# Kernel optimization log

Measured on AMD Instinct MI355X. Metric: run time of the kernel, lower is better.

Reference implementation:

```python
import jax, jax.numpy as jnp
import numpy as np

D_MODEL = 1024
NUM_HEADS = 16
D_K = D_MODEL // NUM_HEADS


def setup_inputs() -> dict:
    key = jax.random.key(0)
    ks = jax.random.split(key, 9)
    s = 1.0 / np.sqrt(D_MODEL)
    x = jax.random.normal(ks[0], (4, 2048, D_MODEL), dtype=jnp.float32)
    Wq = jax.random.uniform(ks[1], (D_MODEL, D_MODEL), jnp.float32, -s, s)
    bq = jax.random.uniform(ks[2], (D_MODEL,), jnp.float32, -s, s)
    Wk = jax.random.uniform(ks[3], (D_MODEL, D_MODEL), jnp.float32, -s, s)
    bk = jax.random.uniform(ks[4], (D_MODEL,), jnp.float32, -s, s)
    Wv = jax.random.uniform(ks[5], (D_MODEL, D_MODEL), jnp.float32, -s, s)
    bv = jax.random.uniform(ks[6], (D_MODEL,), jnp.float32, -s, s)
    Wo = jax.random.uniform(ks[7], (D_MODEL, D_MODEL), jnp.float32, -s, s)
    bo = jax.random.uniform(ks[8], (D_MODEL,), jnp.float32, -s, s)
    return {"x": x, "Wq": Wq, "bq": bq, "Wk": Wk, "bk": bk,
            "Wv": Wv, "bv": bv, "Wo": Wo, "bo": bo}


def reference(x, Wq, bq, Wk, bk, Wv, bv, Wo, bo):
    B, S, _ = x.shape
    # project and split heads: [B,S,D] -> [B,H,S,dk]
    def heads(W, b):
        return (x @ W + b).reshape(B, S, NUM_HEADS, D_K).transpose(0, 2, 1, 3)
    q = heads(Wq, bq)
    k = heads(Wk, bk)
    v = heads(Wv, bv)
    scores = jnp.einsum('bhqd,bhkd->bhqk', q, k) / jnp.sqrt(jnp.float32(D_K))
    attn = jax.nn.softmax(scores, axis=-1)
    out = jnp.einsum('bhqk,bhkd->bhqd', attn, v)
    out = out.transpose(0, 2, 1, 3).reshape(B, S, D_MODEL)
    return out @ Wo + bo
```

## Files before the change

### kernel.cpp

```cpp
#include <hip/hip_runtime.h>
#include <hip/hip_bf16.h>

#define D_MODEL 1024
#define NUM_HEADS 16
#define D_K 64
#define B_SZ 4
#define SEQ 2048
#define SCALE_Q 0.180336881f

typedef short bf16x8 __attribute__((ext_vector_type(8)));
typedef float f32x4 __attribute__((ext_vector_type(4)));
typedef unsigned short u16;

__device__ __forceinline__ unsigned cvtpk(float a, float b) {
    unsigned r;
    asm("v_cvt_pk_bf16_f32 %0, %1, %2" : "=v"(r) : "v"(a), "v"(b));
    return r;
}
__device__ __forceinline__ u16 f2bf(float f) {
    return (u16)cvtpk(f, f);
}
__device__ __forceinline__ float exp2a(float x) {
    float r;
    asm("v_exp_f32 %0, %1" : "=v"(r) : "v"(x));
    return r;
}
__device__ __forceinline__ float max3f(float a, float b, float c) {
    float r;
    asm("v_max3_f32 %0, %1, %2, %3" : "=v"(r) : "v"(a), "v"(b), "v"(c));
    return r;
}
__device__ __forceinline__ void gload_lds16(const u16* g, u16* l) {
    __builtin_amdgcn_global_load_lds(
        (const __attribute__((address_space(1))) unsigned int*)g,
        (__attribute__((address_space(3))) unsigned int*)l, 16, 0, 0);
}

__global__ __launch_bounds__(256) void prep_all(
    const float* __restrict__ xin, u16* __restrict__ xbf,
    const float* __restrict__ W0, const float* __restrict__ W1,
    const float* __restrict__ W2, const float* __restrict__ W3,
    u16* __restrict__ Wt)
{
    __shared__ float tile[64][65];
    const int t = threadIdx.x;
    if (blockIdx.x < 1024) {
        const int n8 = (B_SZ * SEQ * D_MODEL) / 8;
        for (int i = blockIdx.x * 256 + t; i < n8; i += 1024 * 256) {
            float4 a = ((const float4*)xin)[(size_t)i * 2];
            float4 b = ((const float4*)xin)[(size_t)i * 2 + 1];
            uint4 o;
            o.x = cvtpk(a.x, a.y);
            o.y = cvtpk(a.z, a.w);
            o.z = cvtpk(b.x, b.y);
            o.w = cvtpk(b.z, b.w);
            ((uint4*)xbf)[i] = o;
        }
        return;
    }
    const int id = blockIdx.x - 1024;
    const int z  = id >> 8;
    const int by = (id >> 4) & 15;
    const int bx = id & 15;
    const float* W = z == 0 ? W0 : z == 1 ? W1 : z == 2 ? W2 : W3;
    u16* out = Wt + (size_t)z * D_MODEL * D_MODEL;
    const int k0 = by * 64;
    const int n0 = bx * 64;
    #pragma unroll
    for (int it = 0; it < 4; ++it) {
        int idx = it * 256 + t;
        int r = idx >> 4;
        int c = (idx & 15) * 4;
        float4 v = *(const float4*)(W + (size_t)(k0 + r) * D_MODEL + n0 + c);
        tile[r][c + 0] = v.x; tile[r][c + 1] = v.y;
        tile[r][c + 2] = v.z; tile[r][c + 3] = v.w;
    }
    __syncthreads();
    #pragma unroll
    for (int it = 0; it < 2; ++it) {
        int idx = it * 256 + t;
        int r = idx >> 3;
        int c = (idx & 7) * 8;
        uint4 o;
        o.x = cvtpk(tile[c + 0][r], tile[c + 1][r]);
        o.y = cvtpk(tile[c + 2][r], tile[c + 3][r]);
        o.z = cvtpk(tile[c + 4][r], tile[c + 5][r]);
        o.w = cvtpk(tile[c + 6][r], tile[c + 7][r]);
        *(uint4*)(out + (size_t)(n0 + r) * D_MODEL + k0 + c) = o;
    }
}

__global__ __launch_bounds__(256) void gemm_qkv(
    const u16* __restrict__ A, const u16* __restrict__ Wt,
    const float* __restrict__ bq, const float* __restrict__ bk,
    const float* __restrict__ bv, u16* __restrict__ Yb)
{
    __shared__ u16 As[2][128][64];
    __shared__ u16 Bs[2][128][64];
    const int t    = threadIdx.x;
    const int lane = t & 63;
    const int wv   = t >> 6;
    const int wm   = wv >> 1, wn = wv & 1;
    const int g    = lane >> 4;
    const int lr   = lane & 15;
    const int fid  = blockIdx.y * 24 + blockIdx.x;
    const int oid  = (fid & 7) * 192 + (fid >> 3);
    const int m0   = (oid / 24) * 128;
    const int n0   = (oid % 24) * 128;
    const int K    = D_MODEL;

    const int srow = lane >> 3;
    const int scol = (lane & 7) * 8;

    f32x4 acc[4][4];
    #pragma unroll
    for (int i = 0; i < 4; ++i)
        #pragma unroll
        for (int j = 0; j < 4; ++j)
            acc[i][j] = (f32x4){0.f, 0.f, 0.f, 0.f};

    #pragma unroll
    for (int it = 0; it < 4; ++it) {
        const int r = wv * 32 + it * 8;
        gload_lds16(A  + (size_t)(m0 + r + srow) * K + scol, &As[0][r][0]);
        gload_lds16(Wt + (size_t)(n0 + r + srow) * K + scol, &Bs[0][r][0]);
    }

    for (int k0 = 0; k0 < K; k0 += 64) {
        const int cur = (k0 >> 6) & 1;
        __syncthreads();
        if (k0 + 64 < K) {
            const int nb = cur ^ 1;
            #pragma unroll
            for (int it = 0; it < 4; ++it) {
                const int r = wv * 32 + it * 8;
                gload_lds16(A  + (size_t)(m0 + r + srow) * K + k0 + 64 + scol, &As[nb][r][0]);
                gload_lds16(Wt + (size_t)(n0 + r + srow) * K + k0 + 64 + scol, &Bs[nb][r][0]);
            }
        }
        #pragma unroll
        for (int s = 0; s < 2; ++s) {
            bf16x8 af[4], bfr[4];
            #pragma unroll
            for (int mt = 0; mt < 4; ++mt)
                af[mt] = *(const bf16x8*)(&As[cur][wm * 64 + mt * 16 + lr][g * 8 + s * 32]);
            #pragma unroll
            for (int nt = 0; nt < 4; ++nt)
                bfr[nt] = *(const bf16x8*)(&Bs[cur][wn * 64 + nt * 16 + lr][g * 8 + s * 32]);
            #pragma unroll
            for (int mt = 0; mt < 4; ++mt)
                #pragma unroll
                for (int nt = 0; nt < 4; ++nt)
                    acc[mt][nt] = __builtin_amdgcn_mfma_f32_16x16x32_bf16(
                        af[mt], bfr[nt], acc[mt][nt], 0, 0, 0);
        }
    }

    const int which = n0 >> 10;
    const float scale = (which == 0) ? SCALE_Q : 1.0f;
    const float* bp = (which == 0) ? bq : (which == 1) ? bk : bv;
    u16* dst = Yb + (size_t)which * ((size_t)B_SZ * SEQ * D_MODEL);

    float bv4[4];
    #pragma unroll
    for (int nt = 0; nt < 4; ++nt)
        bv4[nt] = bp[((n0 + wn * 64 + nt * 16 + lr) & 1023)];

    #pragma unroll
    for (int mt = 0; mt < 4; ++mt) {
        #pragma unroll
        for (int nt = 0; nt < 4; ++nt) {
            float v4[4];
            #pragma unroll
            for (int r = 0; r < 4; ++r) v4[r] = (acc[mt][nt][r] + bv4[nt]) * scale;
            const int mbase = m0 + wm * 64 + mt * 16 + g * 4;
            const int nn = (n0 + wn * 64 + nt * 16 + lr) & 1023;
            const int h = nn >> 6, d = nn & 63;
            const int bb = mbase >> 11, s2 = mbase & 2047;
            if (which == 2) {
                const int z  = s2 & 63;
                const int zp = (z & 32) + 8 * ((z & 15) >> 2) + 4 * ((z >> 4) & 1);
                const int col = zp ^ ((d & 7) << 3);
                uint2 o;
                o.x = cvtpk(v4[0], v4[1]);
                o.y = cvtpk(v4[2], v4[3]);
                *(uint2*)&dst[(((size_t)(bb * NUM_HEADS + h) * D_K + d) * SEQ) + (s2 & ~63) + col] = o;
            } else {
                #pragma unroll
                for (int r = 0; r < 4; ++r) {
                    const int s2r = s2 + r;
                    const int dd = (which == 1) ? (d ^ ((s2r & 7) << 3)) : d;
                    dst[(((size_t)(bb * NUM_HEADS + h) * SEQ) + s2r) * D_K + dd] = f2bf(v4[r]);
                }
            }
        }
    }
}

__global__ __launch_bounds__(256) void gemm_o(
    const u16* __restrict__ A, const u16* __restrict__ Wt,
    const float* __restrict__ bias, float* __restrict__ Y)
{
    __shared__ u16 As[2][128][64];
    __shared__ u16 Bs[2][128][64];
    const int t    = threadIdx.x;
    const int lane = t & 63;
    const int wv   = t >> 6;
    const int wm   = wv >> 1, wn = wv & 1;
    const int g    = lane >> 4;
    const int lr   = lane & 15;
    const int fid  = blockIdx.y * 8 + blockIdx.x;
    const int oid  = (fid & 7) * 64 + (fid >> 3);
    const int m0   = (oid >> 3) * 128;
    const int n0   = (oid & 7) * 128;
    const int K    = D_MODEL;

    const int srow = lane >> 3;
    const int scol = (lane & 7) * 8;

    f32x4 acc[4][4];
    #pragma unroll
    for (int i = 0; i < 4; ++i)
        #pragma unroll
        for (int j = 0; j < 4; ++j)
            acc[i][j] = (f32x4){0.f, 0.f, 0.f, 0.f};

    #pragma unroll
    for (int it = 0; it < 4; ++it) {
        const int r = wv * 32 + it * 8;
        gload_lds16(A  + (size_t)(m0 + r + srow) * K + scol, &As[0][r][0]);
        gload_lds16(Wt + (size_t)(n0 + r + srow) * K + scol, &Bs[0][r][0]);
    }

    for (int k0 = 0; k0 < K; k0 += 64) {
        const int cur = (k0 >> 6) & 1;
        __syncthreads();
        if (k0 + 64 < K) {
            const int nb = cur ^ 1;
            #pragma unroll
            for (int it = 0; it < 4; ++it) {
                const int r = wv * 32 + it * 8;
                gload_lds16(A  + (size_t)(m0 + r + srow) * K + k0 + 64 + scol, &As[nb][r][0]);
                gload_lds16(Wt + (size_t)(n0 + r + srow) * K + k0 + 64 + scol, &Bs[nb][r][0]);
            }
        }
        #pragma unroll
        for (int s = 0; s < 2; ++s) {
            bf16x8 af[4], bfr[4];
            #pragma unroll
            for (int mt = 0; mt < 4; ++mt)
                af[mt] = *(const bf16x8*)(&As[cur][wm * 64 + mt * 16 + lr][g * 8 + s * 32]);
            #pragma unroll
            for (int nt = 0; nt < 4; ++nt)
                bfr[nt] = *(const bf16x8*)(&Bs[cur][wn * 64 + nt * 16 + lr][g * 8 + s * 32]);
            #pragma unroll
            for (int mt = 0; mt < 4; ++mt)
                #pragma unroll
                for (int nt = 0; nt < 4; ++nt)
                    acc[mt][nt] = __builtin_amdgcn_mfma_f32_16x16x32_bf16(
                        af[mt], bfr[nt], acc[mt][nt], 0, 0, 0);
        }
    }

    float bv4[4];
    #pragma unroll
    for (int nt = 0; nt < 4; ++nt) bv4[nt] = bias[n0 + wn * 64 + nt * 16 + lr];

    #pragma unroll
    for (int mt = 0; mt < 4; ++mt)
        #pragma unroll
        for (int nt = 0; nt < 4; ++nt)
            #pragma unroll
            for (int r = 0; r < 4; ++r) {
                const int m = m0 + wm * 64 + mt * 16 + g * 4 + r;
                const int n = n0 + wn * 64 + nt * 16 + lr;
                Y[(size_t)m * D_MODEL + n] = acc[mt][nt][r] + bv4[nt];
            }
}

__global__ __launch_bounds__(512, 4) void attn_mfma(
    const u16* __restrict__ Q, const u16* __restrict__ Kb,
    const u16* __restrict__ Vt, u16* __restrict__ ctx)
{
    __shared__ u16 Ks[2][128][64];
    __shared__ u16 Vs[2][64][128];
    const int t    = threadIdx.x;
    const int lane = t & 63;
    const int w    = t >> 6;
    const int g    = lane >> 4;
    const int lr   = lane & 15;
    const int fid  = blockIdx.x + (blockIdx.y << 3) + (blockIdx.z << 7);
    const int oid  = (fid & 7) * 64 + (fid >> 3);
    const int qt   = oid & 7;
    const int h    = (oid >> 3) & 15;
    const int b    = oid >> 7;
    const size_t hoff = ((size_t)b * NUM_HEADS + h) * SEQ * D_K;

    bf16x8 qf[2][2];
    #pragma unroll
    for (int u = 0; u < 2; ++u) {
        const int q = qt * 256 + w * 32 + u * 16 + lr;
        qf[u][0] = *(const bf16x8*)(Q + hoff + (size_t)q * D_K + g * 8);
        qf[u][1] = *(const bf16x8*)(Q + hoff + (size_t)q * D_K + g * 8 + 32);
    }

    const int krow = w * 16 + (lane >> 3);
    const int kcol = (lane & 7) * 8;
    const u16* ksrc = Kb + hoff + (size_t)krow * D_K + kcol;
    const int vrow = w * 8 + (lane >> 4);
    const int vcol = (lane & 15) * 8;
    const u16* vsrc = Vt + hoff + (size_t)vrow * SEQ + vcol;

    const int xm = (lr & 7) << 3;

    float mrun[2]  = {0.f, 0.f};
    float lpart[2] = {0.f, 0.f};
    f32x4 acc_o[2][4];
    #pragma unroll
    for (int u = 0; u < 2; ++u)
        #pragma unroll
        for (int n = 0; n < 4; ++n) acc_o[u][n] = (f32x4){0.f, 0.f, 0.f, 0.f};

    gload_lds16(ksrc,               &Ks[0][w * 16][0]);
    gload_lds16(ksrc + 8 * D_K,     &Ks[0][w * 16 + 8][0]);
    gload_lds16(vsrc,               &Vs[0][w * 8][0]);
    gload_lds16(vsrc + 4 * SEQ,     &Vs[0][w * 8 + 4][0]);

    int bu = 0;
    for (int kt = 0; kt < SEQ / 128; ++kt) {
        __syncthreads();
        if (kt + 1 < SEQ / 128) {
            const size_t kv0 = (size_t)(kt + 1) * 128;
            const int nb = bu ^ 1;
            gload_lds16(ksrc + kv0 * D_K,       &Ks[nb][w * 16][0]);
            gload_lds16(ksrc + (kv0 + 8) * D_K, &Ks[nb][w * 16 + 8][0]);
            gload_lds16(vsrc + kv0,             &Vs[nb][w * 8][0]);
            gload_lds16(vsrc + 4 * SEQ + kv0,   &Vs[nb][w * 8 + 4][0]);
        }

        #pragma unroll
        for (int hv = 0; hv < 2; ++hv) {
            f32x4 sc[2][4];
            #pragma unroll
            for (int u = 0; u < 2; ++u) {
                const f32x4 mi = {-mrun[u], -mrun[u], -mrun[u], -mrun[u]};
                #pragma unroll
                for (int mt = 0; mt < 4; ++mt) sc[u][mt] = mi;
            }
            __builtin_amdgcn_s_setprio(1);
            #pragma unroll
            for (int s = 0; s < 2; ++s)
                #pragma unroll
                for (int mt = 0; mt < 4; ++mt) {
                    bf16x8 kf = *(const bf16x8*)(
                        &Ks[bu][hv * 64 + mt * 16 + lr][(g * 8 + s * 32) ^ xm]);
                    sc[0][mt] = __builtin_amdgcn_mfma_f32_16x16x32_bf16(kf, qf[0][s], sc[0][mt], 0, 0, 0);
                    sc[1][mt] = __builtin_amdgcn_mfma_f32_16x16x32_bf16(kf, qf[1][s], sc[1][mt], 0, 0, 0);
                }
            __builtin_amdgcn_s_setprio(0);

            union { bf16x8 v; unsigned u[4]; } pa[2][2];
            #pragma unroll
            for (int u = 0; u < 2; ++u) {
                float t0 = max3f(sc[u][0][0], sc[u][0][1], sc[u][0][2]);
                float t1 = max3f(sc[u][0][3], sc[u][1][0], sc[u][1][1]);
                float t2 = max3f(sc[u][1][2], sc[u][1][3], sc[u][2][0]);
                float t3 = max3f(sc[u][2][1], sc[u][2][2], sc[u][2][3]);
                float t4 = max3f(sc[u][3][0], sc[u][3][1], sc[u][3][2]);
                float tmax = fmaxf(max3f(t0, t1, t2), max3f(t3, t4, sc[u][3][3]));

                if (!__all(tmax <= 8.0f)) {
                    float rowmax = fmaxf(tmax, __shfl_xor(tmax, 16));
                    rowmax = fmaxf(rowmax, __shfl_xor(rowmax, 32));
                    const float excess = fmaxf(rowmax, 0.0f);
                    const float alpha = exp2a(-excess);
                    mrun[u] += excess;
                    lpart[u] *= alpha;
                    float ar[4];
                    #pragma unroll
                    for (int r = 0; r < 4; ++r) ar[r] = __shfl(alpha, g * 4 + r);
                    #pragma unroll
                    for (int n = 0; n < 4; ++n) {
                        f32x4 v = acc_o[u][n];
                        #pragma unroll
                        for (int r = 0; r < 4; ++r) v[r] *= ar[r];
                        acc_o[u][n] = v;
                    }
                    #pragma unroll
                    for (int mt = 0; mt < 4; ++mt)
                        #pragma unroll
                        for (int r = 0; r < 4; ++r) sc[u][mt][r] -= excess;
                }

                float lsum = 0.f;
                #pragma unroll
                for (int mt = 0; mt < 4; ++mt)
                    #pragma unroll
                    for (int r = 0; r < 4; ++r) {
                        const float e = exp2a(sc[u][mt][r]);
                        sc[u][mt][r] = e;
                        lsum += e;
                    }
                lpart[u] += lsum;

                #pragma unroll
                for (int s = 0; s < 2; ++s) {
                    pa[u][s].u[0] = cvtpk(sc[u][2 * s][0],     sc[u][2 * s][1]);
                    pa[u][s].u[1] = cvtpk(sc[u][2 * s][2],     sc[u][2 * s][3]);
                    pa[u][s].u[2] = cvtpk(sc[u][2 * s + 1][0], sc[u][2 * s + 1][1]);
                    pa[u][s].u[3] = cvtpk(sc[u][2 * s + 1][2], sc[u][2 * s + 1][3]);
                }
            }

            __builtin_amdgcn_s_setprio(1);
            #pragma unroll
            for (int s = 0; s < 2; ++s)
                #pragma unroll
                for (int n = 0; n < 4; ++n) {
                    bf16x8 vf = *(const bf16x8*)(
                        &Vs[bu][16 * n + lr][hv * 64 + ((32 * s + 8 * g) ^ xm)]);
                    acc_o[0][n] = __builtin_amdgcn_mfma_f32_16x16x32_bf16(pa[0][s].v, vf, acc_o[0][n], 0, 0, 0);
                    acc_o[1][n] = __builtin_amdgcn_mfma_f32_16x16x32_bf16(pa[1][s].v, vf, acc_o[1][n], 0, 0, 0);
                }
            __builtin_amdgcn_s_setprio(0);
        }
        bu ^= 1;
    }

    #pragma unroll
    for (int u = 0; u < 2; ++u) {
        float l = lpart[u];
        l += __shfl_xor(l, 16);
        l += __shfl_xor(l, 32);
        const float linv = 1.0f / l;
        float lr4[4];
        #pragma unroll
        for (int r = 0; r < 4; ++r) lr4[r] = __shfl(linv, g * 4 + r);
        #pragma unroll
        for (int n = 0; n < 4; ++n)
            #pragma unroll
            for (int r = 0; r < 4; ++r) {
                const int qrow = qt * 256 + w * 32 + u * 16 + 4 * g + r;
                ctx[((size_t)b * SEQ + qrow) * D_MODEL + h * D_K + 16 * n + lr] =
                    f2bf(acc_o[u][n][r] * lr4[r]);
            }
    }
}

extern "C" void kernel_launch(void* const* d_in, const int* in_sizes, int n_in,
                              void* d_out, int out_size, void* d_ws, size_t ws_size,
                              hipStream_t stream)
{
    const float* x  = (const float*)d_in[0];
    const float* Wq = (const float*)d_in[1];
    const float* bq = (const float*)d_in[2];
    const float* Wk = (const float*)d_in[3];
    const float* bk = (const float*)d_in[4];
    const float* Wv = (const float*)d_in[5];
    const float* bv = (const float*)d_in[6];
    const float* Wo = (const float*)d_in[7];
    const float* bo = (const float*)d_in[8];
    float* out = (float*)d_out;

    char* ws = (char*)d_ws;
    const size_t MB = 1024 * 1024;
    u16* xbf  = (u16*)(ws);
    u16* Wt   = (u16*)(ws + 16 * MB);
    u16* Qbf  = (u16*)(ws + 24 * MB);
    u16* ctxb = (u16*)(ws + 72 * MB);
    u16* Kbf  = Qbf + (size_t)B_SZ * SEQ * D_MODEL;
    u16* Vtw  = Kbf + (size_t)B_SZ * SEQ * D_MODEL;

    prep_all<<<2048, 256, 0, stream>>>(x, xbf, Wq, Wk, Wv, Wo, Wt);

    gemm_qkv<<<dim3(3 * D_MODEL / 128, (B_SZ * SEQ) / 128), 256, 0, stream>>>(
        xbf, Wt, bq, bk, bv, Qbf);

    attn_mfma<<<dim3(SEQ / 256, NUM_HEADS, B_SZ), 512, 0, stream>>>(Qbf, Kbf, Vtw, ctxb);

    gemm_o<<<dim3(D_MODEL / 128, (B_SZ * SEQ) / 128), 256, 0, stream>>>(
        ctxb, Wt + 3 * (size_t)D_MODEL * D_MODEL, bo, out);
}
```

Measured before the change: 194.6 us.

## Pre-swizzle bf16 operands in global memory and use 8-wave GEMM blocks

The producers of the GEMM operands now write them with an XOR swizzle on 16-byte chunks. This covers the x conversion, the weight transpose and the attention context store, and it lets the LDS fragment reads in both GEMMs pick banks without conflicts. The GEMM kernels move from 4 to 8 waves per 128x128 tile with a 2x4 wave grid, so each wave holds a 64x32 accumulator. The sync placement changes, and the grouped block-order remap for L2 locality is dropped. This trades lower per-wave register pressure and more latency hiding for smaller per-wave fragment reuse and possibly worse L2 reuse.

```diff
diff --git a/kernel.cpp b/kernel.cpp
--- a/kernel.cpp
+++ b/kernel.cpp
@@ -54,7 +54,8 @@
             o.y = cvtpk(a.z, a.w);
             o.z = cvtpk(b.x, b.y);
             o.w = cvtpk(b.z, b.w);
-            ((uint4*)xbf)[i] = o;
+            const int j = i ^ ((i >> 7) & 7);
+            ((uint4*)xbf)[j] = o;
         }
         return;
     }
@@ -86,11 +87,12 @@
         o.y = cvtpk(tile[c + 2][r], tile[c + 3][r]);
         o.z = cvtpk(tile[c + 4][r], tile[c + 5][r]);
         o.w = cvtpk(tile[c + 6][r], tile[c + 7][r]);
-        *(uint4*)(out + (size_t)(n0 + r) * D_MODEL + k0 + c) = o;
-    }
-}
-
-__global__ __launch_bounds__(256) void gemm_qkv(
+        const int csw = (((idx & 7) ^ (r & 7)) * 8);
+        *(uint4*)(out + (size_t)(n0 + r) * D_MODEL + k0 + csw) = o;
+    }
+}
+
+__global__ __launch_bounds__(512) void gemm_qkv(
     const u16* __restrict__ A, const u16* __restrict__ Wt,
     const float* __restrict__ bq, const float* __restrict__ bk,
     const float* __restrict__ bv, u16* __restrict__ Yb)
@@ -99,61 +101,62 @@
     __shared__ u16 Bs[2][128][64];
     const int t    = threadIdx.x;
     const int lane = t & 63;
-    const int wv   = t >> 6;
-    const int wm   = wv >> 1, wn = wv & 1;
+    const int wid  = t >> 6;
+    const int wm   = wid >> 2;
+    const int wn   = wid & 3;
     const int g    = lane >> 4;
     const int lr   = lane & 15;
-    const int fid  = blockIdx.y * 24 + blockIdx.x;
-    const int oid  = (fid & 7) * 192 + (fid >> 3);
-    const int m0   = (oid / 24) * 128;
-    const int n0   = (oid % 24) * 128;
+    const int m0   = blockIdx.y * 128;
+    const int n0   = blockIdx.x * 128;
     const int K    = D_MODEL;
-
-    const int srow = lane >> 3;
-    const int scol = (lane & 7) * 8;
-
-    f32x4 acc[4][4];
+    const int xm   = (lr & 7) << 3;
+
+    const int srow8 = lane >> 3;
+    const int scol  = (lane & 7) * 8;
+
+    f32x4 acc[4][2];
     #pragma unroll
     for (int i = 0; i < 4; ++i)
         #pragma unroll
-        for (int j = 0; j < 4; ++j)
+        for (int j = 0; j < 2; ++j)
             acc[i][j] = (f32x4){0.f, 0.f, 0.f, 0.f};
 
     #pragma unroll
-    for (int it = 0; it < 4; ++it) {
-        const int r = wv * 32 + it * 8;
-        gload_lds16(A  + (size_t)(m0 + r + srow) * K + scol, &As[0][r][0]);
-        gload_lds16(Wt + (size_t)(n0 + r + srow) * K + scol, &Bs[0][r][0]);
-    }
+    for (int it = 0; it < 2; ++it) {
+        const int seg = it * 8 + wid;
+        gload_lds16(A  + (size_t)(m0 + seg * 8 + srow8) * K + scol, &As[0][seg * 8][0]);
+        gload_lds16(Wt + (size_t)(n0 + seg * 8 + srow8) * K + scol, &Bs[0][seg * 8][0]);
+    }
+    __syncthreads();
 
     for (int k0 = 0; k0 < K; k0 += 64) {
         const int cur = (k0 >> 6) & 1;
-        __syncthreads();
         if (k0 + 64 < K) {
             const int nb = cur ^ 1;
             #pragma unroll
-            for (int it = 0; it < 4; ++it) {
-                const int r = wv * 32 + it * 8;
-                gload_lds16(A  + (size_t)(m0 + r + srow) * K + k0 + 64 + scol, &As[nb][r][0]);
-                gload_lds16(Wt + (size_t)(n0 + r + srow) * K + k0 + 64 + scol, &Bs[nb][r][0]);
+            for (int it = 0; it < 2; ++it) {
+                const int seg = it * 8 + wid;
+                gload_lds16(A  + (size_t)(m0 + seg * 8 + srow8) * K + k0 + 64 + scol, &As[nb][seg * 8][0]);
+                gload_lds16(Wt + (size_t)(n0 + seg * 8 + srow8) * K + k0 + 64 + scol, &Bs[nb][seg * 8][0]);
             }
         }
         #pragma unroll
         for (int s = 0; s < 2; ++s) {
-            bf16x8 af[4], bfr[4];
+            bf16x8 af[4], bfr[2];
             #pragma unroll
             for (int mt = 0; mt < 4; ++mt)
-                af[mt] = *(const bf16x8*)(&As[cur][wm * 64 + mt * 16 + lr][g * 8 + s * 32]);
-            #pragma unroll
-            for (int nt = 0; nt < 4; ++nt)
-                bfr[nt] = *(const bf16x8*)(&Bs[cur][wn * 64 + nt * 16 + lr][g * 8 + s * 32]);
+                af[mt] = *(const bf16x8*)(&As[cur][wm * 64 + mt * 16 + lr][(g * 8 + s * 32) ^ xm]);
+            #pragma unroll
+            for (int nt = 0; nt < 2; ++nt)
+                bfr[nt] = *(const bf16x8*)(&Bs[cur][wn * 32 + nt * 16 + lr][(g * 8 + s * 32) ^ xm]);
             #pragma unroll
             for (int mt = 0; mt < 4; ++mt)
                 #pragma unroll
-                for (int nt = 0; nt < 4; ++nt)
+                for (int nt = 0; nt < 2; ++nt)
                     acc[mt][nt] = __builtin_amdgcn_mfma_f32_16x16x32_bf16(
                         af[mt], bfr[nt], acc[mt][nt], 0, 0, 0);
         }
+        __syncthreads();
     }
 
     const int which = n0 >> 10;
@@ -161,20 +164,20 @@
     const float* bp = (which == 0) ? bq : (which == 1) ? bk : bv;
     u16* dst = Yb + (size_t)which * ((size_t)B_SZ * SEQ * D_MODEL);
 
-    float bv4[4];
-    #pragma unroll
-    for (int nt = 0; nt < 4; ++nt)
-        bv4[nt] = bp[((n0 + wn * 64 + nt * 16 + lr) & 1023)];
+    float bv2[2];
+    #pragma unroll
+    for (int nt = 0; nt < 2; ++nt)
+        bv2[nt] = bp[((n0 + wn * 32 + nt * 16 + lr) & 1023)];
 
     #pragma unroll
     for (int mt = 0; mt < 4; ++mt) {
         #pragma unroll
-        for (int nt = 0; nt < 4; ++nt) {
+        for (int nt = 0; nt < 2; ++nt) {
             float v4[4];
             #pragma unroll
-            for (int r = 0; r < 4; ++r) v4[r] = (acc[mt][nt][r] + bv4[nt]) * scale;
+            for (int r = 0; r < 4; ++r) v4[r] = (acc[mt][nt][r] + bv2[nt]) * scale;
             const int mbase = m0 + wm * 64 + mt * 16 + g * 4;
-            const int nn = (n0 + wn * 64 + nt * 16 + lr) & 1023;
+            const int nn = (n0 + wn * 32 + nt * 16 + lr) & 1023;
             const int h = nn >> 6, d = nn & 63;
             const int bb = mbase >> 11, s2 = mbase & 2047;
             if (which == 2) {
@@ -197,7 +200,7 @@
     }
 }
 
-__global__ __launch_bounds__(256) void gemm_o(
+__global__ __launch_bounds__(512) void gemm_o(
     const u16* __restrict__ A, const u16* __restrict__ Wt,
     const float* __restrict__ bias, float* __restrict__ Y)
 {
@@ -205,76 +208,77 @@
     __shared__ u16 Bs[2][128][64];
     const int t    = threadIdx.x;
     const int lane = t & 63;
-    const int wv   = t >> 6;
-    const int wm   = wv >> 1, wn = wv & 1;
+    const int wid  = t >> 6;
+    const int wm   = wid >> 2;
+    const int wn   = wid & 3;
     const int g    = lane >> 4;
     const int lr   = lane & 15;
-    const int fid  = blockIdx.y * 8 + blockIdx.x;
-    const int oid  = (fid & 7) * 64 + (fid >> 3);
-    const int m0   = (oid >> 3) * 128;
-    const int n0   = (oid & 7) * 128;
+    const int m0   = blockIdx.y * 128;
+    const int n0   = blockIdx.x * 128;
     const int K    = D_MODEL;
-
-    const int srow = lane >> 3;
-    const int scol = (lane & 7) * 8;
-
-    f32x4 acc[4][4];
+    const int xm   = (lr & 7) << 3;
+
+    const int srow8 = lane >> 3;
+    const int scol  = (lane & 7) * 8;
+
+    f32x4 acc[4][2];
     #pragma unroll
     for (int i = 0; i < 4; ++i)
         #pragma unroll
-        for (int j = 0; j < 4; ++j)
+        for (int j = 0; j < 2; ++j)
             acc[i][j] = (f32x4){0.f, 0.f, 0.f, 0.f};
 
     #pragma unroll
-    for (int it = 0; it < 4; ++it) {
-        const int r = wv * 32 + it * 8;
-        gload_lds16(A  + (size_t)(m0 + r + srow) * K + scol, &As[0][r][0]);
-        gload_lds16(Wt + (size_t)(n0 + r + srow) * K + scol, &Bs[0][r][0]);
-    }
+    for (int it = 0; it < 2; ++it) {
+        const int seg = it * 8 + wid;
+        gload_lds16(A  + (size_t)(m0 + seg * 8 + srow8) * K + scol, &As[0][seg * 8][0]);
+        gload_lds16(Wt + (size_t)(n0 + seg * 8 + srow8) * K + scol, &Bs[0][seg * 8][0]);
+    }
+    __syncthreads();
 
     for (int k0 = 0; k0 < K; k0 += 64) {
         const int cur = (k0 >> 6) & 1;
-        __syncthreads();
         if (k0 + 64 < K) {
             const int nb = cur ^ 1;
             #pragma unroll
-            for (int it = 0; it < 4; ++it) {
-                const int r = wv * 32 + it * 8;
-                gload_lds16(A  + (size_t)(m0 + r + srow) * K + k0 + 64 + scol, &As[nb][r][0]);
-                gload_lds16(Wt + (size_t)(n0 + r + srow) * K + k0 + 64 + scol, &Bs[nb][r][0]);
+            for (int it = 0; it < 2; ++it) {
+                const int seg = it * 8 + wid;
+                gload_lds16(A  + (size_t)(m0 + seg * 8 + srow8) * K + k0 + 64 + scol, &As[nb][seg * 8][0]);
+                gload_lds16(Wt + (size_t)(n0 + seg * 8 + srow8) * K + k0 + 64 + scol, &Bs[nb][seg * 8][0]);
             }
         }
         #pragma unroll
         for (int s = 0; s < 2; ++s) {
-            bf16x8 af[4], bfr[4];
+            bf16x8 af[4], bfr[2];
             #pragma unroll
             for (int mt = 0; mt < 4; ++mt)
-                af[mt] = *(const bf16x8*)(&As[cur][wm * 64 + mt * 16 + lr][g * 8 + s * 32]);
-            #pragma unroll
-            for (int nt = 0; nt < 4; ++nt)
-                bfr[nt] = *(const bf16x8*)(&Bs[cur][wn * 64 + nt * 16 + lr][g * 8 + s * 32]);
+                af[mt] = *(const bf16x8*)(&As[cur][wm * 64 + mt * 16 + lr][(g * 8 + s * 32) ^ xm]);
+            #pragma unroll
+            for (int nt = 0; nt < 2; ++nt)
+                bfr[nt] = *(const bf16x8*)(&Bs[cur][wn * 32 + nt * 16 + lr][(g * 8 + s * 32) ^ xm]);
             #pragma unroll
             for (int mt = 0; mt < 4; ++mt)
                 #pragma unroll
-                for (int nt = 0; nt < 4; ++nt)
+                for (int nt = 0; nt < 2; ++nt)
                     acc[mt][nt] = __builtin_amdgcn_mfma_f32_16x16x32_bf16(
                         af[mt], bfr[nt], acc[mt][nt], 0, 0, 0);
         }
-    }
-
-    float bv4[4];
-    #pragma unroll
-    for (int nt = 0; nt < 4; ++nt) bv4[nt] = bias[n0 + wn * 64 + nt * 16 + lr];
+        __syncthreads();
+    }
+
+    float bv2[2];
+    #pragma unroll
+    for (int nt = 0; nt < 2; ++nt) bv2[nt] = bias[n0 + wn * 32 + nt * 16 + lr];
 
     #pragma unroll
     for (int mt = 0; mt < 4; ++mt)
         #pragma unroll
-        for (int nt = 0; nt < 4; ++nt)
+        for (int nt = 0; nt < 2; ++nt)
             #pragma unroll
             for (int r = 0; r < 4; ++r) {
                 const int m = m0 + wm * 64 + mt * 16 + g * 4 + r;
-                const int n = n0 + wn * 64 + nt * 16 + lr;
-                Y[(size_t)m * D_MODEL + n] = acc[mt][nt][r] + bv4[nt];
+                const int n = n0 + wn * 32 + nt * 16 + lr;
+                Y[(size_t)m * D_MODEL + n] = acc[mt][nt][r] + bv2[nt];
             }
 }
 
@@ -441,7 +445,8 @@
             #pragma unroll
             for (int r = 0; r < 4; ++r) {
                 const int qrow = qt * 256 + w * 32 + u * 16 + 4 * g + r;
-                ctx[((size_t)b * SEQ + qrow) * D_MODEL + h * D_K + 16 * n + lr] =
+                const int col  = (h * D_K + 16 * n + lr) ^ ((qrow & 7) << 3);
+                ctx[((size_t)b * SEQ + qrow) * D_MODEL + col] =
                     f2bf(acc_o[u][n][r] * lr4[r]);
             }
     }
@@ -473,11 +478,11 @@
 
     prep_all<<<2048, 256, 0, stream>>>(x, xbf, Wq, Wk, Wv, Wo, Wt);
 
-    gemm_qkv<<<dim3(3 * D_MODEL / 128, (B_SZ * SEQ) / 128), 256, 0, stream>>>(
+    gemm_qkv<<<dim3(3 * D_MODEL / 128, (B_SZ * SEQ) / 128), 512, 0, stream>>>(
         xbf, Wt, bq, bk, bv, Qbf);
 
     attn_mfma<<<dim3(SEQ / 256, NUM_HEADS, B_SZ), 512, 0, stream>>>(Qbf, Kbf, Vtw, ctxb);
 
-    gemm_o<<<dim3(D_MODEL / 128, (B_SZ * SEQ) / 128), 256, 0, stream>>>(
+    gemm_o<<<dim3(D_MODEL / 128, (B_SZ * SEQ) / 128), 512, 0, stream>>>(
         ctxb, Wt + 3 * (size_t)D_MODEL * D_MODEL, bo, out);
 }
```

New measurement: 169.8 us. -12.7%, faster.
